# Performance work log

Measured on AMD Instinct MI355X. Metric: run time of the kernel, lower is better.

The kernel has to match this reference:

```python
import jax, jax.numpy as jnp
import numpy as np

B, L, D, H, DFF, K, NLVL = 8, 16384, 256, 8, 1024, 1000, 4
HD = D // H            # 32 head dim
NP = HD // 2           # 16 rotary pairs per head
GY, GX, GL = 6, 6, 4   # pairs allocated to y, x, level position dims
SPATIAL_THETA, LEVEL_THETA = 100.0, 10.0


def _freqs(n, theta):
    return theta ** (-jnp.arange(n, dtype=jnp.float32) / n)


def _layer_norm(x, g, b):
    mu = jnp.mean(x, axis=-1, keepdims=True)
    v = jnp.mean(jnp.square(x - mu), axis=-1, keepdims=True)
    return (x - mu) * jax.lax.rsqrt(v + 1e-5) * g + b


def _apply_rope(t, cos, sin):
    # t: [B, K, H, HD]; cos/sin: [B, K, 1, NP] (heads shared)
    tr = t.reshape(t.shape[:-1] + (NP, 2))
    t1, t2 = tr[..., 0], tr[..., 1]
    return jnp.stack([t1 * cos - t2 * sin, t1 * sin + t2 * cos], axis=-1).reshape(t.shape)


def setup_inputs() -> dict:
    key = jax.random.key(0)
    ks = jax.random.split(key, 12)
    N = B * L
    s = 0.02
    batch_idx = jnp.repeat(jnp.arange(B, dtype=jnp.int32), L)
    spat = jax.random.randint(ks[3], (2, N), 0, 32, dtype=jnp.int32)
    lvl = jax.random.randint(ks[4], (1, N), 0, NLVL, dtype=jnp.int32)
    return {
        "queries": jax.random.normal(ks[0], (N, D), jnp.float32),
        "query_batch_offsets": jnp.arange(B + 1, dtype=jnp.int32) * L,
        "token_predicted_salience_score": jax.random.uniform(ks[1], (N,), jnp.float32),
        "token_electron_scores": jax.random.uniform(ks[2], (N,), jnp.float32),
        "query_spatial_indices": jnp.concatenate([batch_idx[None], spat, lvl], axis=0),
        "stacked_feature_maps": jnp.zeros((1,), jnp.float32),  # unused (neighborhood attn off)
        "level_spatial_shapes": jnp.array([[256, 256], [128, 128], [64, 64], [32, 32]], jnp.int32),
        "Wqkv": jax.random.normal(ks[5], (D, 3 * D), jnp.float32) * s,
        "Wo": jax.random.normal(ks[6], (D, D), jnp.float32) * s,
        "ln1_g": jnp.ones((D,), jnp.float32), "ln1_b": jnp.zeros((D,), jnp.float32),
        "W1": jax.random.normal(ks[7], (D, DFF), jnp.float32) * s,
        "b1": jnp.zeros((DFF,), jnp.float32),
        "W2": jax.random.normal(ks[8], (DFF, D), jnp.float32) * s,
        "b2": jnp.zeros((D,), jnp.float32),
        "ln2_g": jnp.ones((D,), jnp.float32), "ln2_b": jnp.zeros((D,), jnp.float32),
    }


def reference(queries, query_batch_offsets, token_predicted_salience_score,
              query_spatial_indices, stacked_feature_maps, level_spatial_shapes,
              token_electron_scores, Wqkv, Wo, ln1_g, ln1_b, W1, b1, W2, b2, ln2_g, ln2_b):
    # --- per-batch top-k salience selection (equal-length fast path) ---
    scores = (token_electron_scores + token_predicted_salience_score).reshape(B, L)
    _, idx = jax.lax.top_k(jax.lax.stop_gradient(scores), K)           # [B, K]
    topk_indices = (idx + query_batch_offsets[:-1, None]).reshape(-1)  # [B*K]

    # --- gather selected tokens ---
    x = queries[topk_indices]                          # [B*K, D]
    sp = query_spatial_indices[:, topk_indices]        # [4, B*K]
    pos = sp[1:3].T.astype(jnp.float32)                # [B*K, 2] (y, x)
    lvl = sp[3]
    shapes_f = level_spatial_shapes.astype(jnp.float32)
    pos = pos * (shapes_f[0][None, :] / shapes_f[lvl])  # rescale to finest level
    lvl_f = lvl.astype(jnp.float32)

    ang = jnp.concatenate([
        pos[:, 0:1] * _freqs(GY, SPATIAL_THETA)[None, :],
        pos[:, 1:2] * _freqs(GX, SPATIAL_THETA)[None, :],
        lvl_f[:, None] * _freqs(GL, LEVEL_THETA)[None, :],
    ], axis=-1)                                        # [B*K, NP]
    cos = jnp.cos(ang).reshape(B, K, 1, NP)
    sin = jnp.sin(ang).reshape(B, K, 1, NP)

    # --- pre-norm RoPE self-attention over selected tokens ---
    h = _layer_norm(x, ln1_g, ln1_b)
    qkv = h @ Wqkv                                     # [B*K, 3D]
    q, k, v = [t.reshape(B, K, H, HD) for t in jnp.split(qkv, 3, axis=-1)]
    q = _apply_rope(q, cos, sin)
    k = _apply_rope(k, cos, sin)
    att = jnp.einsum('bqhd,bkhd->bhqk', q, k) / jnp.sqrt(jnp.float32(HD))
    att = jax.nn.softmax(att, axis=-1)
    out = jnp.einsum('bhqk,bkhd->bqhd', att, v).reshape(B * K, D) @ Wo
    sa_out = x + out

    # --- scatter (index_copy) back ---
    queries = queries.at[topk_indices].set(sa_out)

    # --- pre-norm FFN on all tokens ---
    h2 = _layer_norm(queries, ln2_g, ln2_b)
    queries = queries + (jax.nn.gelu(h2 @ W1 + b1) @ W2 + b2)
    return queries
```

## Files before the change

### kernel.cpp

```cpp
#include <hip/hip_runtime.h>
#include <hip/hip_bf16.h>
#include <math.h>

#define B_   8
#define L_   16384
#define D_   256
#define H_   8
#define DFF_ 1024
#define KSEL 1000
#define NTOK (B_*KSEL)
#define NALL (B_*L_)
#define HD_  32
#define NP_  16

typedef float f32x4 __attribute__((ext_vector_type(4)));
typedef short s16x8 __attribute__((ext_vector_type(8)));
typedef unsigned short u16x8 __attribute__((ext_vector_type(8)));
typedef unsigned short u16x4 __attribute__((ext_vector_type(4)));

static __device__ __forceinline__ unsigned short f2bf(float f) {
  __bf16 b = (__bf16)f;
  return __builtin_bit_cast(unsigned short, b);
}
static __device__ __forceinline__ float bf2f(unsigned short h) {
  return __uint_as_float(((unsigned)h) << 16);
}
static __device__ __forceinline__ f32x4 mfma_bf16(s16x8 a, s16x8 b, f32x4 c) {
  return __builtin_amdgcn_mfma_f32_16x16x32_bf16(a, b, c, 0, 0, 0);
}

__global__ __launch_bounds__(256) void transpose_all(
    const float* Wqkv, const float* Wo, const float* W1, const float* W2,
    unsigned short* Wqkvt, unsigned short* Wot, unsigned short* W1t, unsigned short* W2t) {
  __shared__ float tile[32][33];
  int bid = blockIdx.x;
  const float* src; unsigned short* dst; int K, N, tl;
  if (bid < 192)      { src = Wqkv; dst = Wqkvt; K = 256;  N = 768;  tl = bid; }
  else if (bid < 256) { src = Wo;   dst = Wot;   K = 256;  N = 256;  tl = bid - 192; }
  else if (bid < 512) { src = W1;   dst = W1t;   K = 256;  N = 1024; tl = bid - 256; }
  else                { src = W2;   dst = W2t;   K = 1024; N = 256;  tl = bid - 512; }
  int ntx = N >> 5;
  int n0 = (tl % ntx) * 32, k0 = (tl / ntx) * 32;
  int tx = threadIdx.x & 31, ty = threadIdx.x >> 5;
#pragma unroll
  for (int r = 0; r < 32; r += 8)
    tile[ty + r][tx] = src[(size_t)(k0 + ty + r) * N + n0 + tx];
  __syncthreads();
#pragma unroll
  for (int r = 0; r < 32; r += 8)
    dst[(size_t)(n0 + ty + r) * K + k0 + tx] = f2bf(tile[tx][ty + r]);
}

__global__ __launch_bounds__(1024) void topk_kernel(const float* es, const float* ss, int* out_idx) {
  __shared__ int wsum[16];
  __shared__ int chunk_base;
  int b = blockIdx.x;
  int t = threadIdx.x;
  int lane = t & 63, w = t >> 6;
  int base = b * L_;
  unsigned kreg[16];
#pragma unroll
  for (int ci = 0; ci < 16; ++ci) {
    int i = ci * 1024 + t;
    float f = es[base + i] + ss[base + i];
    unsigned u = __float_as_uint(f);
    kreg[ci] = (u & 0x80000000u) ? ~u : (u | 0x80000000u);
  }
  unsigned v = 0;
  for (int bit = 31; bit >= 0; --bit) {
    unsigned cand = v | (1u << bit);
    int c = 0;
#pragma unroll
    for (int ci = 0; ci < 16; ++ci) c += (kreg[ci] >= cand) ? 1 : 0;
    for (int m = 1; m < 64; m <<= 1) c += __shfl_xor(c, m);
    if (lane == 0) wsum[w] = c;
    __syncthreads();
    int tot = 0;
#pragma unroll
    for (int j = 0; j < 16; ++j) tot += wsum[j];
    if (tot >= KSEL) v = cand;
    __syncthreads();
  }
  if (t == 0) chunk_base = 0;
  __syncthreads();
  for (int pass = 0; pass < 2; ++pass) {
    for (int ci = 0; ci < 16; ++ci) {
      bool pred = (pass == 0) ? (kreg[ci] > v) : (kreg[ci] == v);
      unsigned long long mask = __ballot(pred);
      if (lane == 0) wsum[w] = __popcll(mask);
      __syncthreads();
      int wbase = chunk_base;
      for (int j = 0; j < w; ++j) wbase += wsum[j];
      if (pred) {
        int pos = wbase + __popcll(mask & ((1ull << lane) - 1ull));
        if (pos < KSEL) out_idx[b * KSEL + pos] = base + ci * 1024 + t;
      }
      __syncthreads();
      if (t == 0) { int tt = 0; for (int j = 0; j < 16; ++j) tt += wsum[j]; chunk_base += tt; }
      __syncthreads();
    }
  }
}

__global__ __launch_bounds__(256) void gather_ln_rope(
    const float* queries, const int* idx, const int* spat, const int* shapes,
    const float* g1, const float* b1ln, unsigned short* h, float* cosb, float* sinb) {
  int tok = blockIdx.x;
  int t = threadIdx.x;
  int gidx = idx[tok];
  float x = queries[(size_t)gidx * D_ + t];
  float s1 = x, s2 = x * x;
  for (int m = 1; m < 64; m <<= 1) { s1 += __shfl_xor(s1, m); s2 += __shfl_xor(s2, m); }
  __shared__ float p1[4], p2[4];
  int w = t >> 6;
  if ((t & 63) == 0) { p1[w] = s1; p2[w] = s2; }
  __syncthreads();
  float tot  = p1[0] + p1[1] + p1[2] + p1[3];
  float tot2 = p2[0] + p2[1] + p2[2] + p2[3];
  float mu = tot / D_;
  float var = tot2 / D_ - mu * mu;
  float rs = 1.0f / sqrtf(var + 1e-5f);
  h[(size_t)tok * D_ + t] = f2bf((x - mu) * rs * g1[t] + b1ln[t]);
  if (t < NP_) {
    int yy = spat[1*(size_t)NALL + gidx];
    int xx = spat[2*(size_t)NALL + gidx];
    int lv = spat[3*(size_t)NALL + gidx];
    float ang;
    if (t < 6) {
      float sc = (float)shapes[0] / (float)shapes[lv*2+0];
      ang = (float)yy * sc * powf(100.0f, -(float)t / 6.0f);
    } else if (t < 12) {
      float sc = (float)shapes[1] / (float)shapes[lv*2+1];
      ang = (float)xx * sc * powf(100.0f, -(float)(t-6) / 6.0f);
    } else {
      ang = (float)lv * powf(10.0f, -(float)(t-12) / 4.0f);
    }
    cosb[tok*NP_ + t] = cosf(ang);
    sinb[tok*NP_ + t] = sinf(ang);
  }
}

__global__ __launch_bounds__(256) void qkv_gemm(
    const unsigned short* h, const unsigned short* Wt,
    unsigned short* qh, unsigned short* kh, unsigned short* vh) {
  __shared__ unsigned short a_lds[64][264];
  int m0 = blockIdx.y * 64;
  int n0 = blockIdx.x * 128;
  int t = threadIdx.x, lane = t & 63, w = t >> 6;
  int lm = lane & 15, lg = lane >> 4;
  for (int it = 0; it < 8; ++it) {
    int c = it*256 + t;
    int row = c >> 5, off = (c & 31) * 8;
    *(uint4*)&a_lds[row][off] = *(const uint4*)&h[(size_t)(m0+row)*D_ + off];
  }
  __syncthreads();
  f32x4 acc[8];
#pragma unroll
  for (int i = 0; i < 8; ++i) acc[i] = (f32x4){0.f,0.f,0.f,0.f};
#pragma unroll
  for (int ks = 0; ks < 8; ++ks) {
    s16x8 a = *(const s16x8*)&a_lds[w*16 + lm][ks*32 + lg*8];
#pragma unroll
    for (int nt = 0; nt < 8; ++nt) {
      s16x8 bb = *(const s16x8*)&Wt[(size_t)(n0 + nt*16 + lm)*D_ + ks*32 + lg*8];
      acc[nt] = mfma_bf16(a, bb, acc[nt]);
    }
  }
#pragma unroll
  for (int i = 0; i < 4; ++i) {
    int row = w*16 + lg*4 + i;
    int tok = m0 + row;
    int b = tok / 1000, tk = tok - b*1000;
#pragma unroll
    for (int nt = 0; nt < 8; ++nt) {
      int col = n0 + nt*16 + lm;
      int part = col >> 8;
      int within = col & 255;
      int head = within >> 5, d = within & 31;
      unsigned short* dst = part == 0 ? qh : (part == 1 ? kh : vh);
      dst[(size_t)((b*H_ + head)*1000 + tk)*HD_ + d] = f2bf(acc[nt][i]);
    }
  }
}

__global__ __launch_bounds__(256) void attn_kernel(
    const unsigned short* qh, const unsigned short* kh, const unsigned short* vh,
    const float* cosb, const float* sinb, unsigned short* obuf) {
  __shared__ unsigned short k_lds[64][40];
  __shared__ unsigned short vt_lds[32][72];
  __shared__ unsigned short p_lds[4][16][72];
  int bh = blockIdx.y;
  int b = bh >> 3, hh = bh & 7;
  int q0 = blockIdx.x * 64;
  int t = threadIdx.x, lane = t & 63, w = t >> 6;
  int lm = lane & 15, lg = lane >> 4;

  int qrow = q0 + w*16 + lm;
  int qtk = qrow < 999 ? qrow : 999;
  int qtokg = b*1000 + qtk;
  s16x8 qf;
  {
    u16x8 raw = *(const u16x8*)&qh[(size_t)(bh*1000 + qtk)*HD_ + lg*8];
    f32x4 c4 = *(const f32x4*)&cosb[(size_t)qtokg*NP_ + lg*4];
    f32x4 s4 = *(const f32x4*)&sinb[(size_t)qtokg*NP_ + lg*4];
#pragma unroll
    for (int m = 0; m < 4; ++m) {
      float t1 = bf2f(raw[2*m]), t2 = bf2f(raw[2*m+1]);
      float e = t1*c4[m] - t2*s4[m];
      float o = t1*s4[m] + t2*c4[m];
      qf[2*m]   = (short)f2bf(e);
      qf[2*m+1] = (short)f2bf(o);
    }
  }

  float m_run[4], l_run[4];
  f32x4 o_acc[2];
#pragma unroll
  for (int i = 0; i < 4; ++i) { m_run[i] = -1e30f; l_run[i] = 0.f; }
  o_acc[0] = (f32x4){0.f,0.f,0.f,0.f};
  o_acc[1] = (f32x4){0.f,0.f,0.f,0.f};

  for (int ch = 0; ch < 16; ++ch) {
    int c0 = ch * 64;
    __syncthreads();
    for (int it = 0; it < 4; ++it) {
      int pi = it*256 + t;
      int key = pi >> 4, pp = pi & 15;
      int tk = c0 + key; tk = tk < 999 ? tk : 999;
      int tokg = b*1000 + tk;
      unsigned raw = *(const unsigned*)&kh[(size_t)(bh*1000 + tk)*HD_ + pp*2];
      float cc = cosb[(size_t)tokg*NP_ + pp], scn = sinb[(size_t)tokg*NP_ + pp];
      float t1 = bf2f((unsigned short)(raw & 0xFFFFu));
      float t2 = bf2f((unsigned short)(raw >> 16));
      float e = t1*cc - t2*scn, od = t1*scn + t2*cc;
      unsigned outp = (unsigned)f2bf(e) | ((unsigned)f2bf(od) << 16);
      *(unsigned*)&k_lds[key][pp*2] = outp;
    }
    for (int it = 0; it < 4; ++it) {
      int e2 = it*256 + t;
      int key = e2 >> 4, dp = e2 & 15;
      int tk = c0 + key; tk = tk < 999 ? tk : 999;
      unsigned raw = *(const unsigned*)&vh[(size_t)(bh*1000 + tk)*HD_ + dp*2];
      vt_lds[dp*2][key]   = (unsigned short)(raw & 0xFFFFu);
      vt_lds[dp*2+1][key] = (unsigned short)(raw >> 16);
    }
    __syncthreads();
    f32x4 sacc[4];
#pragma unroll
    for (int nt = 0; nt < 4; ++nt) {
      sacc[nt] = (f32x4){0.f,0.f,0.f,0.f};
      s16x8 bb = *(const s16x8*)&k_lds[nt*16 + lm][lg*8];
      sacc[nt] = mfma_bf16(qf, bb, sacc[nt]);
    }
    const float scale = 0.17677669529663687f;
#pragma unroll
    for (int nt = 0; nt < 4; ++nt) {
      int col = c0 + nt*16 + lm;
      bool valid = col < 1000;
#pragma unroll
      for (int i = 0; i < 4; ++i) sacc[nt][i] = valid ? sacc[nt][i]*scale : -1e30f;
    }
#pragma unroll
    for (int i = 0; i < 4; ++i) {
      float mx = fmaxf(fmaxf(sacc[0][i], sacc[1][i]), fmaxf(sacc[2][i], sacc[3][i]));
      for (int m = 1; m < 16; m <<= 1) mx = fmaxf(mx, __shfl_xor(mx, m));
      float mn = fmaxf(m_run[i], mx);
      float alpha = __expf(m_run[i] - mn);
      float rsum = 0.f;
#pragma unroll
      for (int nt = 0; nt < 4; ++nt) { float p = __expf(sacc[nt][i] - mn); sacc[nt][i] = p; rsum += p; }
      for (int m = 1; m < 16; m <<= 1) rsum += __shfl_xor(rsum, m);
      l_run[i] = l_run[i]*alpha + rsum;
      m_run[i] = mn;
      o_acc[0][i] *= alpha; o_acc[1][i] *= alpha;
    }
#pragma unroll
    for (int nt = 0; nt < 4; ++nt)
#pragma unroll
      for (int i = 0; i < 4; ++i)
        p_lds[w][lg*4 + i][nt*16 + lm] = f2bf(sacc[nt][i]);
#pragma unroll
    for (int kk = 0; kk < 2; ++kk) {
      s16x8 pf = *(const s16x8*)&p_lds[w][lm][kk*32 + lg*8];
#pragma unroll
      for (int dt = 0; dt < 2; ++dt) {
        s16x8 vf = *(const s16x8*)&vt_lds[dt*16 + lm][kk*32 + lg*8];
        o_acc[dt] = mfma_bf16(pf, vf, o_acc[dt]);
      }
    }
  }
#pragma unroll
  for (int i = 0; i < 4; ++i) {
    int qr = q0 + w*16 + lg*4 + i;
    if (qr < 1000) {
      float innorm = 1.0f / l_run[i];
      int tokg = b*1000 + qr;
#pragma unroll
      for (int dt = 0; dt < 2; ++dt)
        obuf[(size_t)tokg*D_ + hh*HD_ + dt*16 + lm] = f2bf(o_acc[dt][i] * innorm);
    }
  }
}

__global__ __launch_bounds__(256) void wo_scatter(
    const unsigned short* obuf, const unsigned short* Wot,
    const float* queries, const int* idx, float* sa, int* slot_of) {
  __shared__ unsigned short a_lds[64][264];
  int m0 = blockIdx.x * 64;
  int t = threadIdx.x, lane = t & 63, w = t >> 6;
  int lm = lane & 15, lg = lane >> 4;
  for (int it = 0; it < 8; ++it) {
    int c = it*256 + t;
    int row = c >> 5, off = (c & 31) * 8;
    *(uint4*)&a_lds[row][off] = *(const uint4*)&obuf[(size_t)(m0+row)*D_ + off];
  }
  if (t < 64) { int tok = m0 + t; slot_of[idx[tok]] = tok; }
  __syncthreads();
  f32x4 acc[16];
#pragma unroll
  for (int i = 0; i < 16; ++i) acc[i] = (f32x4){0.f,0.f,0.f,0.f};
#pragma unroll
  for (int ks = 0; ks < 8; ++ks) {
    s16x8 a = *(const s16x8*)&a_lds[w*16 + lm][ks*32 + lg*8];
#pragma unroll
    for (int nt = 0; nt < 16; ++nt) {
      s16x8 bb = *(const s16x8*)&Wot[(size_t)(nt*16 + lm)*D_ + ks*32 + lg*8];
      acc[nt] = mfma_bf16(a, bb, acc[nt]);
    }
  }
#pragma unroll
  for (int i = 0; i < 4; ++i) {
    int row = w*16 + lg*4 + i;
    int tok = m0 + row;
    int g = idx[tok];
#pragma unroll
    for (int nt = 0; nt < 16; ++nt) {
      int col = nt*16 + lm;
      sa[(size_t)tok*D_ + col] = queries[(size_t)g*D_ + col] + acc[nt][i];
    }
  }
}

__global__ __launch_bounds__(512, 4) void ffn_kernel(
    const float* queries, const float* sa, const int* slot_of,
    const unsigned short* W1t, const unsigned short* W2t,
    const float* b1, const float* b2, const float* g2, const float* bb2,
    float* out) {
  __shared__ unsigned short h2[64*256];
  __shared__ unsigned short c1[2*64*128];
  int m0 = blockIdx.x * 64;
  int t = threadIdx.x, lane = t & 63, w = t >> 6;
  int lm = lane & 15, lg = lane >> 4;
  int x4 = (lm & 7) << 4;

  {
    f32x4 g2v  = *(const f32x4*)&g2[lane*4];
    f32x4 bb2v = *(const f32x4*)&bb2[lane*4];
#pragma unroll
    for (int rr = 0; rr < 8; ++rr) {
      int row = w*8 + rr;
      int grow = m0 + row;
      int slot = slot_of[grow];
      const float* xb = (slot >= 0) ? (sa + (size_t)slot * D_) : (queries + (size_t)grow * D_);
      f32x4 x = *(const f32x4*)&xb[lane*4];
      float s1 = x[0]+x[1]+x[2]+x[3];
      float s2 = x[0]*x[0]+x[1]*x[1]+x[2]*x[2]+x[3]*x[3];
      for (int m = 1; m < 64; m <<= 1) { s1 += __shfl_xor(s1, m); s2 += __shfl_xor(s2, m); }
      float mu = s1 * (1.0f/D_);
      float rs = __builtin_amdgcn_rsqf(s2 * (1.0f/D_) - mu*mu + 1e-5f);
      u16x4 hv;
#pragma unroll
      for (int j = 0; j < 4; ++j) hv[j] = f2bf((x[j]-mu)*rs*g2v[j] + bb2v[j]);
      *(u16x4*)((char*)h2 + row*512 + ((lane*8) ^ ((row & 7) << 4))) = hv;
    }
  }

  f32x4 acc2[2][4];
#pragma unroll
  for (int at = 0; at < 2; ++at)
#pragma unroll
    for (int rt = 0; rt < 4; ++rt) acc2[at][rt] = (f32x4){0.f,0.f,0.f,0.f};

  const char* h2c = (const char*)h2;
  char* c1base = (char*)c1;
  const unsigned short* w1base = W1t + (size_t)(w*16 + lm) * D_ + lg*8;
  const unsigned short* w2base = W2t + (size_t)(w*32 + lm) * DFF_ + lg*8;

  auto run_g1 = [&](int hc, int buf) {
    f32x4 acc1[4];
#pragma unroll
    for (int rt = 0; rt < 4; ++rt) acc1[rt] = (f32x4){0.f,0.f,0.f,0.f};
    const unsigned short* w1p = w1base + (size_t)hc * 128 * D_;
#pragma unroll
    for (int ks = 0; ks < 8; ++ks) {
      s16x8 wa = *(const s16x8*)(w1p + ks*32);
#pragma unroll
      for (int rt = 0; rt < 4; ++rt) {
        s16x8 f = *(const s16x8*)(h2c + (rt*16 + lm)*512 + ((ks*64 + lg*16) ^ x4));
        acc1[rt] = mfma_bf16(wa, f, acc1[rt]);
      }
    }
    f32x4 b1v = *(const f32x4*)&b1[hc*128 + w*16 + lg*4];
    char* cb = c1base + buf * 16384;
#pragma unroll
    for (int rt = 0; rt < 4; ++rt) {
      u16x4 pv;
#pragma unroll
      for (int i = 0; i < 4; ++i) {
        float xv = acc1[rt][i] + b1v[i];
        float z = 0.7978845608028654f * xv * fmaf(xv*xv, 0.044715f, 1.0f);
        float e = __builtin_amdgcn_exp2f(z * -2.885390081777927f);
        float rcp = __builtin_amdgcn_rcpf(1.0f + e);
        float th = fmaf(-2.0f*e, rcp, 1.0f);
        float y = 0.5f * xv;
        y = fmaf(y, th, y);
        pv[i] = f2bf(y);
      }
      *(u16x4*)(cb + (rt*16 + lm)*256 + ((w*32 + lg*8) ^ x4)) = pv;
    }
  };
  auto run_g2 = [&](int hc, int buf) {
    const char* cb = c1base + buf * 16384;
#pragma unroll
    for (int ks = 0; ks < 4; ++ks) {
      s16x8 wa0 = *(const s16x8*)(w2base + hc*128 + ks*32);
      s16x8 wa1 = *(const s16x8*)(w2base + (size_t)16*DFF_ + hc*128 + ks*32);
#pragma unroll
      for (int rt = 0; rt < 4; ++rt) {
        s16x8 f = *(const s16x8*)(cb + (rt*16 + lm)*256 + ((ks*64 + lg*16) ^ x4));
        acc2[0][rt] = mfma_bf16(wa0, f, acc2[0][rt]);
        acc2[1][rt] = mfma_bf16(wa1, f, acc2[1][rt]);
      }
    }
  };

  __syncthreads();
  run_g1(0, 0);
  __syncthreads();
  for (int hc = 0; hc < 8; ++hc) {
    if (hc < 7) run_g1(hc + 1, (hc + 1) & 1);
    run_g2(hc, hc & 1);
    __syncthreads();
  }

#pragma unroll
  for (int rt = 0; rt < 4; ++rt) {
    int grow = m0 + rt*16 + lm;
    int slot = slot_of[grow];
    const float* xb = (slot >= 0) ? (sa + (size_t)slot * D_) : (queries + (size_t)grow * D_);
#pragma unroll
    for (int at = 0; at < 2; ++at) {
      int oc = w*32 + at*16 + lg*4;
      f32x4 b2v = *(const f32x4*)&b2[oc];
      f32x4 xv = *(const f32x4*)&xb[oc];
      f32x4 v;
#pragma unroll
      for (int i = 0; i < 4; ++i) v[i] = acc2[at][rt][i] + xv[i] + b2v[i];
      *(f32x4*)&out[(size_t)grow * D_ + oc] = v;
    }
  }
}

extern "C" void kernel_launch(void* const* d_in, const int* in_sizes, int n_in,
                              void* d_out, int out_size, void* d_ws, size_t ws_size,
                              hipStream_t stream) {
  const float* queries = (const float*)d_in[0];
  const float* sal   = (const float*)d_in[2];
  const float* ele   = (const float*)d_in[3];
  const int*   spat  = (const int*)d_in[4];
  const int*   shapes= (const int*)d_in[6];
  const float* Wqkv  = (const float*)d_in[7];
  const float* Wo    = (const float*)d_in[8];
  const float* ln1g  = (const float*)d_in[9];
  const float* ln1b  = (const float*)d_in[10];
  const float* W1    = (const float*)d_in[11];
  const float* b1    = (const float*)d_in[12];
  const float* W2    = (const float*)d_in[13];
  const float* b2    = (const float*)d_in[14];
  const float* ln2g  = (const float*)d_in[15];
  const float* ln2b  = (const float*)d_in[16];
  float* out = (float*)d_out;

  char* ws = (char*)d_ws;
  size_t off = 0;
  auto alloc = [&](size_t bytes) -> void* {
    void* p = ws + off;
    off = (off + bytes + 255) & ~(size_t)255;
    return p;
  };
  int*            idxb  = (int*)alloc((size_t)NTOK * 4);
  unsigned short* h     = (unsigned short*)alloc((size_t)NTOK * D_ * 2);
  float*          cosb  = (float*)alloc((size_t)NTOK * NP_ * 4);
  float*          sinb  = (float*)alloc((size_t)NTOK * NP_ * 4);
  unsigned short* qh    = (unsigned short*)alloc((size_t)NTOK * D_ * 2);
  unsigned short* kh    = (unsigned short*)alloc((size_t)NTOK * D_ * 2);
  unsigned short* vh    = (unsigned short*)alloc((size_t)NTOK * D_ * 2);
  unsigned short* obuf  = (unsigned short*)alloc((size_t)NTOK * D_ * 2);
  unsigned short* Wqkvt = (unsigned short*)alloc((size_t)768 * 256 * 2);
  unsigned short* Wot   = (unsigned short*)alloc((size_t)256 * 256 * 2);
  unsigned short* W1t   = (unsigned short*)alloc((size_t)1024 * 256 * 2);
  unsigned short* W2t   = (unsigned short*)alloc((size_t)256 * 1024 * 2);
  float*          sa    = (float*)alloc((size_t)NTOK * D_ * 4);
  int*            slot  = (int*)alloc((size_t)NALL * 4);

  (void)hipMemsetAsync(slot, 0xFF, (size_t)NALL * 4, stream);
  transpose_all<<<768, 256, 0, stream>>>(Wqkv, Wo, W1, W2, Wqkvt, Wot, W1t, W2t);
  topk_kernel<<<B_, 1024, 0, stream>>>(ele, sal, idxb);
  gather_ln_rope<<<NTOK, 256, 0, stream>>>(queries, idxb, spat, shapes, ln1g, ln1b, h, cosb, sinb);
  qkv_gemm<<<dim3(6, 125), 256, 0, stream>>>(h, Wqkvt, qh, kh, vh);
  attn_kernel<<<dim3(16, 64), 256, 0, stream>>>(qh, kh, vh, cosb, sinb, obuf);
  wo_scatter<<<125, 256, 0, stream>>>(obuf, Wot, queries, idxb, sa, slot);
  ffn_kernel<<<2048, 512, 0, stream>>>(queries, sa, slot, W1t, W2t, b1, b2, ln2g, ln2b, out);
}
```

Measured before the change: 491.0 us.

## Retile FFN kernel to 128-row blocks with 2D warp tiling and larger chunks

The FFN kernel now handles 128 tokens per block instead of 64. Its 8 warps are arranged as a 2x4 grid, so each warp computes a 64x64 output tile, and the hidden dimension is walked in 4 chunks of 256 instead of 8 chunks of 128. The aim is to load each weight fragment once per block for twice as many tokens, roughly halving global/L2 weight traffic, and to raise MFMA work per LDS and global load. The cost is larger accumulator register use and 128 KB of LDS per block, which forces launch bounds down to 2 blocks per SM. It also drops the double-buffered overlap of the two GEMMs in favour of synchronised phases.

```diff
diff --git a/kernel.cpp b/kernel.cpp
--- a/kernel.cpp
+++ b/kernel.cpp
@@ -341,24 +341,26 @@
   }
 }
 
-__global__ __launch_bounds__(512, 4) void ffn_kernel(
+__global__ __launch_bounds__(512, 2) void ffn_kernel(
     const float* queries, const float* sa, const int* slot_of,
     const unsigned short* W1t, const unsigned short* W2t,
     const float* b1, const float* b2, const float* g2, const float* bb2,
     float* out) {
-  __shared__ unsigned short h2[64*256];
-  __shared__ unsigned short c1[2*64*128];
-  int m0 = blockIdx.x * 64;
+  __shared__ unsigned short h2[128*256];
+  __shared__ unsigned short c1[128*256];
+  int m0 = blockIdx.x * 128;
   int t = threadIdx.x, lane = t & 63, w = t >> 6;
   int lm = lane & 15, lg = lane >> 4;
+  int g  = w & 3;
+  int mg = w >> 2;
   int x4 = (lm & 7) << 4;
 
   {
     f32x4 g2v  = *(const f32x4*)&g2[lane*4];
     f32x4 bb2v = *(const f32x4*)&bb2[lane*4];
 #pragma unroll
-    for (int rr = 0; rr < 8; ++rr) {
-      int row = w*8 + rr;
+    for (int rr = 0; rr < 16; ++rr) {
+      int row = w*16 + rr;
       int grow = m0 + row;
       int slot = slot_of[grow];
       const float* xb = (slot >= 0) ? (sa + (size_t)slot * D_) : (queries + (size_t)grow * D_);
@@ -374,88 +376,96 @@
       *(u16x4*)((char*)h2 + row*512 + ((lane*8) ^ ((row & 7) << 4))) = hv;
     }
   }
-
-  f32x4 acc2[2][4];
-#pragma unroll
-  for (int at = 0; at < 2; ++at)
-#pragma unroll
-    for (int rt = 0; rt < 4; ++rt) acc2[at][rt] = (f32x4){0.f,0.f,0.f,0.f};
+  __syncthreads();
+
+  f32x4 acc2[4][4];
+#pragma unroll
+  for (int a = 0; a < 4; ++a)
+#pragma unroll
+    for (int m = 0; m < 4; ++m) acc2[a][m] = (f32x4){0.f,0.f,0.f,0.f};
 
   const char* h2c = (const char*)h2;
-  char* c1base = (char*)c1;
-  const unsigned short* w1base = W1t + (size_t)(w*16 + lm) * D_ + lg*8;
-  const unsigned short* w2base = W2t + (size_t)(w*32 + lm) * DFF_ + lg*8;
-
-  auto run_g1 = [&](int hc, int buf) {
-    f32x4 acc1[4];
-#pragma unroll
-    for (int rt = 0; rt < 4; ++rt) acc1[rt] = (f32x4){0.f,0.f,0.f,0.f};
-    const unsigned short* w1p = w1base + (size_t)hc * 128 * D_;
+  char* c1c = (char*)c1;
+  const unsigned short* w2base = W2t + (size_t)(g*64 + lm) * DFF_ + lg*8;
+
+  for (int ch = 0; ch < 4; ++ch) {
+    f32x4 acc1[4][4];
+#pragma unroll
+    for (int a = 0; a < 4; ++a)
+#pragma unroll
+      for (int m = 0; m < 4; ++m) acc1[a][m] = (f32x4){0.f,0.f,0.f,0.f};
+    const unsigned short* w1p = W1t + (size_t)(ch*256 + g*64 + lm) * D_ + lg*8;
 #pragma unroll
     for (int ks = 0; ks < 8; ++ks) {
-      s16x8 wa = *(const s16x8*)(w1p + ks*32);
-#pragma unroll
-      for (int rt = 0; rt < 4; ++rt) {
-        s16x8 f = *(const s16x8*)(h2c + (rt*16 + lm)*512 + ((ks*64 + lg*16) ^ x4));
-        acc1[rt] = mfma_bf16(wa, f, acc1[rt]);
+      s16x8 wa0 = *(const s16x8*)(w1p + (size_t)( 0*D_) + ks*32);
+      s16x8 wa1 = *(const s16x8*)(w1p + (size_t)(16*D_) + ks*32);
+      s16x8 wa2 = *(const s16x8*)(w1p + (size_t)(32*D_) + ks*32);
+      s16x8 wa3 = *(const s16x8*)(w1p + (size_t)(48*D_) + ks*32);
+#pragma unroll
+      for (int mt = 0; mt < 4; ++mt) {
+        int row = mg*64 + mt*16 + lm;
+        s16x8 hb = *(const s16x8*)(h2c + row*512 + ((ks*64 + lg*16) ^ x4));
+        acc1[0][mt] = mfma_bf16(wa0, hb, acc1[0][mt]);
+        acc1[1][mt] = mfma_bf16(wa1, hb, acc1[1][mt]);
+        acc1[2][mt] = mfma_bf16(wa2, hb, acc1[2][mt]);
+        acc1[3][mt] = mfma_bf16(wa3, hb, acc1[3][mt]);
       }
     }
-    f32x4 b1v = *(const f32x4*)&b1[hc*128 + w*16 + lg*4];
-    char* cb = c1base + buf * 16384;
-#pragma unroll
-    for (int rt = 0; rt < 4; ++rt) {
-      u16x4 pv;
-#pragma unroll
-      for (int i = 0; i < 4; ++i) {
-        float xv = acc1[rt][i] + b1v[i];
-        float z = 0.7978845608028654f * xv * fmaf(xv*xv, 0.044715f, 1.0f);
-        float e = __builtin_amdgcn_exp2f(z * -2.885390081777927f);
-        float rcp = __builtin_amdgcn_rcpf(1.0f + e);
-        float th = fmaf(-2.0f*e, rcp, 1.0f);
-        float y = 0.5f * xv;
-        y = fmaf(y, th, y);
-        pv[i] = f2bf(y);
+    __syncthreads();
+#pragma unroll
+    for (int dt = 0; dt < 4; ++dt) {
+      f32x4 b1v = *(const f32x4*)&b1[ch*256 + g*64 + dt*16 + lg*4];
+#pragma unroll
+      for (int mt = 0; mt < 4; ++mt) {
+        int row = mg*64 + mt*16 + lm;
+        u16x4 pv;
+#pragma unroll
+        for (int i = 0; i < 4; ++i) {
+          float xv = acc1[dt][mt][i] + b1v[i];
+          float z = 0.7978845608028654f * xv * fmaf(xv*xv, 0.044715f, 1.0f);
+          float e = __builtin_amdgcn_exp2f(z * -2.885390081777927f);
+          float rcp = __builtin_amdgcn_rcpf(1.0f + e);
+          float th = fmaf(-2.0f*e, rcp, 1.0f);
+          float y = 0.5f * xv;
+          y = fmaf(y, th, y);
+          pv[i] = f2bf(y);
+        }
+        *(u16x4*)(c1c + row*512 + ((g*128 + dt*32 + lg*8) ^ x4)) = pv;
       }
-      *(u16x4*)(cb + (rt*16 + lm)*256 + ((w*32 + lg*8) ^ x4)) = pv;
-    }
-  };
-  auto run_g2 = [&](int hc, int buf) {
-    const char* cb = c1base + buf * 16384;
-#pragma unroll
-    for (int ks = 0; ks < 4; ++ks) {
-      s16x8 wa0 = *(const s16x8*)(w2base + hc*128 + ks*32);
-      s16x8 wa1 = *(const s16x8*)(w2base + (size_t)16*DFF_ + hc*128 + ks*32);
-#pragma unroll
-      for (int rt = 0; rt < 4; ++rt) {
-        s16x8 f = *(const s16x8*)(cb + (rt*16 + lm)*256 + ((ks*64 + lg*16) ^ x4));
-        acc2[0][rt] = mfma_bf16(wa0, f, acc2[0][rt]);
-        acc2[1][rt] = mfma_bf16(wa1, f, acc2[1][rt]);
+    }
+    __syncthreads();
+    const unsigned short* w2p = w2base + ch*256;
+#pragma unroll
+    for (int kk = 0; kk < 8; ++kk) {
+      s16x8 wa0 = *(const s16x8*)(w2p + (size_t)( 0*DFF_) + kk*32);
+      s16x8 wa1 = *(const s16x8*)(w2p + (size_t)(16*DFF_) + kk*32);
+      s16x8 wa2 = *(const s16x8*)(w2p + (size_t)(32*DFF_) + kk*32);
+      s16x8 wa3 = *(const s16x8*)(w2p + (size_t)(48*DFF_) + kk*32);
+#pragma unroll
+      for (int mt = 0; mt < 4; ++mt) {
+        int row = mg*64 + mt*16 + lm;
+        s16x8 cb = *(const s16x8*)(c1c + row*512 + ((kk*64 + lg*16) ^ x4));
+        acc2[0][mt] = mfma_bf16(wa0, cb, acc2[0][mt]);
+        acc2[1][mt] = mfma_bf16(wa1, cb, acc2[1][mt]);
+        acc2[2][mt] = mfma_bf16(wa2, cb, acc2[2][mt]);
+        acc2[3][mt] = mfma_bf16(wa3, cb, acc2[3][mt]);
       }
     }
-  };
-
-  __syncthreads();
-  run_g1(0, 0);
-  __syncthreads();
-  for (int hc = 0; hc < 8; ++hc) {
-    if (hc < 7) run_g1(hc + 1, (hc + 1) & 1);
-    run_g2(hc, hc & 1);
-    __syncthreads();
-  }
-
-#pragma unroll
-  for (int rt = 0; rt < 4; ++rt) {
-    int grow = m0 + rt*16 + lm;
+  }
+
+#pragma unroll
+  for (int mt = 0; mt < 4; ++mt) {
+    int grow = m0 + mg*64 + mt*16 + lm;
     int slot = slot_of[grow];
     const float* xb = (slot >= 0) ? (sa + (size_t)slot * D_) : (queries + (size_t)grow * D_);
 #pragma unroll
-    for (int at = 0; at < 2; ++at) {
-      int oc = w*32 + at*16 + lg*4;
+    for (int oct = 0; oct < 4; ++oct) {
+      int oc = g*64 + oct*16 + lg*4;
       f32x4 b2v = *(const f32x4*)&b2[oc];
       f32x4 xv = *(const f32x4*)&xb[oc];
       f32x4 v;
 #pragma unroll
-      for (int i = 0; i < 4; ++i) v[i] = acc2[at][rt][i] + xv[i] + b2v[i];
+      for (int i = 0; i < 4; ++i) v[i] = acc2[oct][mt][i] + xv[i] + b2v[i];
       *(f32x4*)&out[(size_t)grow * D_ + oc] = v;
     }
   }
@@ -510,5 +520,5 @@
   qkv_gemm<<<dim3(6, 125), 256, 0, stream>>>(h, Wqkvt, qh, kh, vh);
   attn_kernel<<<dim3(16, 64), 256, 0, stream>>>(qh, kh, vh, cosb, sinb, obuf);
   wo_scatter<<<125, 256, 0, stream>>>(obuf, Wot, queries, idxb, sa, slot);
-  ffn_kernel<<<2048, 512, 0, stream>>>(queries, sa, slot, W1t, W2t, b1, b2, ln2g, ln2b, out);
-}
+  ffn_kernel<<<1024, 512, 0, stream>>>(queries, sa, slot, W1t, W2t, b1, b2, ln2g, ln2b, out);
+}
```

Measured after the change: 552.6 us. 12.5% more time.
